# Kernel tuning notes

Hardware: AMD Instinct MI355X
Metric: run time of the kernel (lower is better)

Reference implementation:

```python
import jax, jax.numpy as jnp
import numpy as np

N_NODES = 100000
N_EDGES = 3200000
N_RELS = 8
F_IN = 64
F_OUT = 64


def setup_inputs() -> dict:
    key = jax.random.key(0)
    k1, k2, k3, k4, k5, k6 = jax.random.split(key, 6)
    X = jax.random.normal(k1, (N_NODES, F_IN), dtype=jnp.float32)
    W = jax.random.normal(k2, (N_RELS, F_IN, F_OUT), dtype=jnp.float32) * 0.1
    A = jax.random.uniform(k3, (N_EDGES,), dtype=jnp.float32)
    src = jax.random.randint(k4, (N_EDGES,), 0, N_NODES, dtype=jnp.int32)
    dst = jax.random.randint(k5, (N_EDGES,), 0, N_NODES, dtype=jnp.int32)
    etype = jax.random.randint(k6, (N_EDGES,), 0, N_RELS, dtype=jnp.int32)
    return {"X": X, "W": W, "A": A, "src": src, "dst": dst, "etype": etype}


def reference(X, W, A, src, dst, etype):
    # RGCN hetero forward: Y[i,fo] = sum_{r,j in N_r(i)} A[r,i,j] * (X[j] @ W[r])[fo]
    # Precompute per-relation transformed features: [R, N, F_out]
    XW = jnp.einsum('nf,rfo->rno', X, W)
    # Gather per-edge message and scale by edge weight: [E, F_out]
    msg = XW[etype, src] * A[:, None]
    # Scatter-add into destination nodes: [N, F_out]
    Y = jax.ops.segment_sum(msg, dst, num_segments=X.shape[0])
    return Y
```

## Files before the change

kernel.cpp:

```cpp
#include <hip/hip_runtime.h>
#include <hip/hip_fp16.h>

#define FDIM 64
#define SB 200
#define P_BLK 1024
#define NB_MAX 400
#define BKT_NODES 256
#define CHUNK_CAP 3200

typedef __attribute__((ext_vector_type(8))) short short8;
typedef __attribute__((ext_vector_type(4))) float float4_;

__device__ __forceinline__ unsigned short f2bf(float x) {
    unsigned u = __float_as_uint(x);
    return (unsigned short)((u + 0x7FFF + ((u >> 16) & 1)) >> 16);
}

__global__ __launch_bounds__(256) void xw_gemm_mfma(
    const float* __restrict__ X, const float* __restrict__ Wmat,
    __half* __restrict__ XWh, int N, int R)
{
    __shared__ unsigned short Wt[4 * 64 * 72];
    const int tid  = threadIdx.x;
    const int lane = tid & 63;
    const int wave = tid >> 6;
    const int quad = lane >> 4;
    const int l15  = lane & 15;
    const int blockBase = blockIdx.x * 256;

    short8 bfrag[4][2];
    bool tvalid[4];
#pragma unroll
    for (int t = 0; t < 4; ++t) {
        const int tb = blockBase + (wave * 4 + t) * 16;
        tvalid[t] = (tb < N);
        if (tvalid[t]) {
            const float* xp = X + (size_t)(tb + l15) * FDIM + quad * 8;
            const float4 x0 = *(const float4*)(xp);
            const float4 x1 = *(const float4*)(xp + 4);
            const float4 x2 = *(const float4*)(xp + 32);
            const float4 x3 = *(const float4*)(xp + 36);
            short8 b0, b1;
            b0[0]=f2bf(x0.x); b0[1]=f2bf(x0.y); b0[2]=f2bf(x0.z); b0[3]=f2bf(x0.w);
            b0[4]=f2bf(x1.x); b0[5]=f2bf(x1.y); b0[6]=f2bf(x1.z); b0[7]=f2bf(x1.w);
            b1[0]=f2bf(x2.x); b1[1]=f2bf(x2.y); b1[2]=f2bf(x2.z); b1[3]=f2bf(x2.w);
            b1[4]=f2bf(x3.x); b1[5]=f2bf(x3.y); b1[6]=f2bf(x3.z); b1[7]=f2bf(x3.w);
            bfrag[t][0] = b0; bfrag[t][1] = b1;
        } else {
            bfrag[t][0] = (short8)(0); bfrag[t][1] = (short8)(0);
        }
    }

    for (int rp = 0; rp < 2; ++rp) {
        __syncthreads();
#pragma unroll
        for (int it = 0; it < 16; ++it) {
            const int idx = it * 256 + tid;
            const int k  = idx & 63;
            const int f4 = (idx >> 6) & 15;
            const int r  = idx >> 10;
            const float4 w = *(const float4*)(Wmat + (((size_t)(rp * 4 + r) * FDIM + k) * FDIM + f4 * 4));
            const int base = (r * 64 + f4 * 4) * 72 + k;
            Wt[base + 0 * 72] = f2bf(w.x);
            Wt[base + 1 * 72] = f2bf(w.y);
            Wt[base + 2 * 72] = f2bf(w.z);
            Wt[base + 3 * 72] = f2bf(w.w);
        }
        __syncthreads();

#pragma unroll
        for (int t = 0; t < 4; ++t) {
            if (!tvalid[t]) continue;
            const int tb = blockBase + (wave * 4 + t) * 16;
            const int node = tb + l15;
#pragma unroll
            for (int r = 0; r < 4; ++r) {
                __half* orow = XWh + ((size_t)(rp * 4 + r) * N + node) * FDIM;
#pragma unroll
                for (int ft = 0; ft < 4; ++ft) {
                    const int f = ft * 16 + l15;
                    const unsigned short* wp = &Wt[(r * 64 + f) * 72 + quad * 8];
                    const short8 a0 = *(const short8*)(wp);
                    const short8 a1 = *(const short8*)(wp + 32);
                    float4_ acc = {0.f, 0.f, 0.f, 0.f};
                    acc = __builtin_amdgcn_mfma_f32_16x16x32_bf16(a0, bfrag[t][0], acc, 0, 0, 0);
                    acc = __builtin_amdgcn_mfma_f32_16x16x32_bf16(a1, bfrag[t][1], acc, 0, 0, 0);
                    const __half2 h01 = __floats2half2_rn(acc[0], acc[1]);
                    const __half2 h23 = __floats2half2_rn(acc[2], acc[3]);
                    uint2 st;
                    st.x = *(const unsigned*)&h01;
                    st.y = *(const unsigned*)&h23;
                    *(uint2*)(orow + ft * 16 + quad * 4) = st;
                }
            }
        }
    }
}

__global__ __launch_bounds__(256) void bin_hist(
    const int* __restrict__ dst, int* __restrict__ cnt, int E, int B, int chunk)
{
    __shared__ int lh[NB_MAX];
    const int p = blockIdx.x, tid = threadIdx.x;
    for (int b = tid; b < B; b += 256) lh[b] = 0;
    __syncthreads();
    const int i0 = p * chunk, iend = min(i0 + chunk, E);
    for (int i = i0 + tid; i < iend; i += 256)
        atomicAdd(&lh[dst[i] >> 8], 1);
    __syncthreads();
    for (int b = tid; b < B; b += 256) cnt[(size_t)b * P_BLK + p] = lh[b];
}

__global__ __launch_bounds__(256) void scan_partial(
    const int* __restrict__ cnt, int* __restrict__ blockSums, int M, int CH)
{
    __shared__ int sh[256];
    const int b = blockIdx.x, tid = threadIdx.x;
    const int i0 = b * CH, iend = min(i0 + CH, M);
    int s = 0;
    for (int i = i0 + tid; i < iend; i += 256) s += cnt[i];
    sh[tid] = s; __syncthreads();
    for (int off = 128; off > 0; off >>= 1) {
        if (tid < off) sh[tid] += sh[tid + off];
        __syncthreads();
    }
    if (tid == 0) blockSums[b] = sh[0];
}

__global__ __launch_bounds__(256) void scan_block(int* blockSums, int nb)
{
    __shared__ int sh[256];
    const int tid = threadIdx.x;
    const int v = (tid < nb) ? blockSums[tid] : 0;
    sh[tid] = v; __syncthreads();
    for (int off = 1; off < 256; off <<= 1) {
        const int t = (tid >= off) ? sh[tid - off] : 0;
        __syncthreads();
        sh[tid] += t;
        __syncthreads();
    }
    if (tid < nb) blockSums[tid] = sh[tid] - v;
}

__global__ __launch_bounds__(64) void scan_final(
    const int* __restrict__ cnt, const int* __restrict__ blockSums,
    int* __restrict__ offs, int M, int CH, int E)
{
    const int b = blockIdx.x, lane = threadIdx.x;
    const int i0 = b * CH, iend = min(i0 + CH, M);
    int carry = blockSums[b];
    for (int t = i0; t < iend; t += 64) {
        const int i = t + lane;
        const int c = (i < iend) ? cnt[i] : 0;
        int v = c;
#pragma unroll
        for (int o = 1; o < 64; o <<= 1) {
            const int u = __shfl_up(v, o, 64);
            if (lane >= o) v += u;
        }
        if (i < iend) offs[i] = carry + v - c;
        carry += __shfl(v, 63, 64);
    }
    if (b == (int)gridDim.x - 1 && lane == 0) offs[M] = E;
}

__global__ __launch_bounds__(256) void bin_scatter(
    const int* __restrict__ src, const int* __restrict__ dst,
    const int* __restrict__ etype, const float* __restrict__ A,
    const int* __restrict__ offs, int2* __restrict__ packed,
    int E, int N, int B, int chunk)
{
    __shared__ int lcnt[NB_MAX];
    __shared__ int lpfx[NB_MAX];
    __shared__ int gb[NB_MAX];
    __shared__ int2 recs[CHUNK_CAP];
    __shared__ unsigned short rbkt[CHUNK_CAP];
    const int p = blockIdx.x, tid = threadIdx.x;
    const int i0 = p * chunk, iend = min(i0 + chunk, E);

    for (int b = tid; b < B; b += 256) lcnt[b] = 0;
    __syncthreads();
    for (int i = i0 + tid; i < iend; i += 256)
        atomicAdd(&lcnt[dst[i] >> 8], 1);
    __syncthreads();

    if (tid < 64) {
        int carry = 0;
        for (int t0 = 0; t0 < B; t0 += 64) {
            const int b = t0 + tid;
            const int c = (b < B) ? lcnt[b] : 0;
            int v = c;
#pragma unroll
            for (int o = 1; o < 64; o <<= 1) {
                const int u = __shfl_up(v, o, 64);
                if (tid >= o) v += u;
            }
            if (b < B) lpfx[b] = carry + v - c;
            carry += __shfl(v, 63, 64);
        }
    }
    __syncthreads();
    for (int b = tid; b < B; b += 256) {
        gb[b] = offs[(size_t)b * P_BLK + p] - lpfx[b];
        lcnt[b] = lpfx[b];
    }
    __syncthreads();

    for (int i = i0 + tid; i < iend; i += 256) {
        const int d = dst[i];
        const int b = d >> 8;
        const int slot = atomicAdd(&lcnt[b], 1);
        recs[slot] = make_int2((etype[i] * N + src[i]) | ((d & 255) << 20),
                               __float_as_int(A[i]));
        rbkt[slot] = (unsigned short)b;
    }
    __syncthreads();

    const int tot = iend - i0;
    for (int s = tid; s < tot; s += 256)
        packed[gb[rbkt[s]] + s] = recs[s];
}

__global__ __launch_bounds__(1024) void bucket_sort(
    const int2* __restrict__ packed, const int* __restrict__ offs,
    int2* __restrict__ sorted, int* __restrict__ nodeOffs, int N, int B, int E)
{
    __shared__ int hist[BKT_NODES];
    __shared__ int pfx[BKT_NODES + 1];
    __shared__ int cur[BKT_NODES];
    const int bkt = blockIdx.x, tid = threadIdx.x;
    const int beg = offs[(size_t)bkt * P_BLK];
    const int end = (bkt + 1 < B) ? offs[(size_t)(bkt + 1) * P_BLK] : E;

    if (tid < BKT_NODES) hist[tid] = 0;
    __syncthreads();
    for (int i = beg + tid; i < end; i += 1024)
        atomicAdd(&hist[(packed[i].x >> 20) & (BKT_NODES - 1)], 1);
    __syncthreads();
    if (tid == 0) {
        int s = 0;
        pfx[0] = 0;
        for (int i = 0; i < BKT_NODES; ++i) { s += hist[i]; pfx[i + 1] = s; }
    }
    __syncthreads();
    if (tid < BKT_NODES) {
        cur[tid] = pfx[tid];
        const int n = bkt * BKT_NODES + tid;
        if (n < N) nodeOffs[n] = beg + pfx[tid];
    }
    if (bkt == B - 1 && tid == 0) nodeOffs[N] = E;
    __syncthreads();
    for (int i = beg + tid; i < end; i += 1024) {
        const int2 rec = packed[i];
        const int dl = (rec.x >> 20) & (BKT_NODES - 1);
        const int pos = atomicAdd(&cur[dl], 1);
        sorted[beg + pos] = rec;
    }
}

__global__ __launch_bounds__(256) void dst_aggregate(
    const __half* __restrict__ XWh, const int* __restrict__ nodeOffs,
    const int2* __restrict__ sorted, float* __restrict__ Y, int N)
{
    const int lane = threadIdx.x & 63;
    const int hid  = lane >> 5;
    const int fl   = lane & 31;
    const int wave = (int)((blockIdx.x * blockDim.x + threadIdx.x) >> 6);
    const int nWaves = (int)((gridDim.x * blockDim.x) >> 6);
    const __half2* XW2 = (const __half2*)XWh;

    for (int d = wave; d < N; d += nWaves) {
        const int beg = nodeOffs[d], end = nodeOffs[d + 1];
        float ax = 0.f, ay = 0.f;
        for (int base = beg; base < end; base += 64) {
            const int idx = base + lane;
            const int2 ka = (idx < end) ? sorted[idx] : make_int2(0, 0);
            const int nb = min(64, end - base);
            const int npair = (nb + 1) >> 1;
            int s = 0;
            for (; s + 8 <= npair; s += 8) {
                int k[8], b[8];
#pragma unroll
                for (int u = 0; u < 8; ++u) {
                    const int j = 2 * (s + u) + hid;
                    k[u] = __shfl(ka.x, j, 64);
                    b[u] = __shfl(ka.y, j, 64);
                }
                __half2 v[8];
#pragma unroll
                for (int u = 0; u < 8; ++u)
                    v[u] = XW2[(size_t)(k[u] & 0xFFFFF) * 32 + fl];
#pragma unroll
                for (int u = 0; u < 8; ++u) {
                    const float2 f = __half22float2(v[u]);
                    const float a = __int_as_float(b[u]);
                    ax += a * f.x; ay += a * f.y;
                }
            }
            for (; s < npair; ++s) {
                const int j = 2 * s + hid;
                const int kk = __shfl(ka.x, j, 64);
                const int bb = __shfl(ka.y, j, 64);
                const __half2 v = XW2[(size_t)(kk & 0xFFFFF) * 32 + fl];
                const float2 f = __half22float2(v);
                const float a = __int_as_float(bb);
                ax += a * f.x; ay += a * f.y;
            }
        }
        ax += __shfl_xor(ax, 32, 64);
        ay += __shfl_xor(ay, 32, 64);
        if (lane < 32) {
            ((float2*)(Y + (size_t)d * FDIM))[fl] = make_float2(ax, ay);
        }
    }
}

extern "C" void kernel_launch(void* const* d_in, const int* in_sizes, int n_in,
                              void* d_out, int out_size, void* d_ws, size_t ws_size,
                              hipStream_t stream)
{
    const float* X     = (const float*)d_in[0];
    const float* Wmat  = (const float*)d_in[1];
    const float* A     = (const float*)d_in[2];
    const int*   src   = (const int*)d_in[3];
    const int*   dst   = (const int*)d_in[4];
    const int*   etype = (const int*)d_in[5];
    float* Y = (float*)d_out;

    const int N = in_sizes[0] / FDIM;
    const int R = in_sizes[1] / (FDIM * FDIM);
    const int E = in_sizes[2];
    (void)n_in; (void)out_size; (void)ws_size;

    const int B = (N + BKT_NODES - 1) / BKT_NODES;
    const int M = B * P_BLK;
    const int chunk = (E + P_BLK - 1) / P_BLK;
    const int CH = (M + SB - 1) / SB;

    char* ws = (char*)d_ws;
    size_t off = 0;
    auto take = [&](size_t bytes) { char* p = ws + off; off = (off + bytes + 255) & ~(size_t)255; return p; };
    __half* XWh      = (__half*)take((size_t)R * N * FDIM * sizeof(__half));
    int2*   packed   = (int2*)  take((size_t)E * sizeof(int2));
    int2*   sorted   = (int2*)  take((size_t)E * sizeof(int2));
    int*    cnt      = (int*)   take((size_t)M * sizeof(int));
    int*    offs     = (int*)   take((size_t)(M + 1) * sizeof(int));
    int*    nodeOffs = (int*)   take((size_t)(N + 1) * sizeof(int));
    int*    bsums    = (int*)   take((size_t)SB * sizeof(int));

    xw_gemm_mfma<<<(N + 255) / 256, 256, 0, stream>>>(X, Wmat, XWh, N, R);

    bin_hist<<<P_BLK, 256, 0, stream>>>(dst, cnt, E, B, chunk);
    scan_partial<<<SB, 256, 0, stream>>>(cnt, bsums, M, CH);
    scan_block<<<1, 256, 0, stream>>>(bsums, SB);
    scan_final<<<SB, 64, 0, stream>>>(cnt, bsums, offs, M, CH, E);
    bin_scatter<<<P_BLK, 256, 0, stream>>>(src, dst, etype, A, offs, packed, E, N, B, chunk);
    bucket_sort<<<B, 1024, 0, stream>>>(packed, offs, sorted, nodeOffs, N, B, E);

    dst_aggregate<<<2048, 256, 0, stream>>>(XWh, nodeOffs, sorted, Y, N);
}
```

Measured before the change: 315.6 us.

## Process four edges per wave step with 8-byte gathers and prefetch next node offsets

The aggregation kernel now splits each wave into four 16-lane groups. Each lane loads four fp16 features (a uint2) per edge, so a wave handles four edges per step instead of two, halving the number of gather iterations. The remainder loop is removed by padding the step count to a multiple of 8, relying on the zeroed padding records (weight 0, index 0). The next node's offsets are prefetched during the current node, and the final reduction takes two xor-shuffles across 16-lane groups before a float4 store.

```diff
diff --git a/kernel.cpp b/kernel.cpp
--- a/kernel.cpp
+++ b/kernel.cpp
@@ -263,55 +263,62 @@
     const int2* __restrict__ sorted, float* __restrict__ Y, int N)
 {
     const int lane = threadIdx.x & 63;
-    const int hid  = lane >> 5;
-    const int fl   = lane & 31;
+    const int el   = lane >> 4;
+    const int fl4  = lane & 15;
     const int wave = (int)((blockIdx.x * blockDim.x + threadIdx.x) >> 6);
     const int nWaves = (int)((gridDim.x * blockDim.x) >> 6);
-    const __half2* XW2 = (const __half2*)XWh;
-
-    for (int d = wave; d < N; d += nWaves) {
-        const int beg = nodeOffs[d], end = nodeOffs[d + 1];
-        float ax = 0.f, ay = 0.f;
+    const __half2* __restrict__ XW2 = (const __half2*)XWh;
+    const unsigned foff = (unsigned)(fl4 << 1);
+
+    int d = wave;
+    if (d >= N) return;
+    int beg = nodeOffs[d];
+    int end = nodeOffs[d + 1];
+
+    while (d < N) {
+        const int dn = d + nWaves;
+        int nbeg = 0, nend = 0;
+        if (dn < N) { nbeg = nodeOffs[dn]; nend = nodeOffs[dn + 1]; }
+
+        float4_ acc = {0.f, 0.f, 0.f, 0.f};
         for (int base = beg; base < end; base += 64) {
             const int idx = base + lane;
             const int2 ka = (idx < end) ? sorted[idx] : make_int2(0, 0);
             const int nb = min(64, end - base);
-            const int npair = (nb + 1) >> 1;
-            int s = 0;
-            for (; s + 8 <= npair; s += 8) {
+            const int nsteps = (((nb + 3) >> 2) + 7) & ~7;
+            for (int s = 0; s < nsteps; s += 8) {
                 int k[8], b[8];
 #pragma unroll
                 for (int u = 0; u < 8; ++u) {
-                    const int j = 2 * (s + u) + hid;
+                    const int j = ((s + u) << 2) + el;
                     k[u] = __shfl(ka.x, j, 64);
                     b[u] = __shfl(ka.y, j, 64);
                 }
-                __half2 v[8];
+                uint2 v[8];
 #pragma unroll
                 for (int u = 0; u < 8; ++u)
-                    v[u] = XW2[(size_t)(k[u] & 0xFFFFF) * 32 + fl];
+                    v[u] = *(const uint2*)(XW2 + ((((unsigned)k[u]) & 0xFFFFFu) << 5) + foff);
 #pragma unroll
                 for (int u = 0; u < 8; ++u) {
-                    const float2 f = __half22float2(v[u]);
                     const float a = __int_as_float(b[u]);
-                    ax += a * f.x; ay += a * f.y;
+                    const float2 f0 = __half22float2(*(const __half2*)&v[u].x);
+                    const float2 f1 = __half22float2(*(const __half2*)&v[u].y);
+                    acc[0] += a * f0.x; acc[1] += a * f0.y;
+                    acc[2] += a * f1.x; acc[3] += a * f1.y;
                 }
             }
-            for (; s < npair; ++s) {
-                const int j = 2 * s + hid;
-                const int kk = __shfl(ka.x, j, 64);
-                const int bb = __shfl(ka.y, j, 64);
-                const __half2 v = XW2[(size_t)(kk & 0xFFFFF) * 32 + fl];
-                const float2 f = __half22float2(v);
-                const float a = __int_as_float(bb);
-                ax += a * f.x; ay += a * f.y;
-            }
-        }
-        ax += __shfl_xor(ax, 32, 64);
-        ay += __shfl_xor(ay, 32, 64);
-        if (lane < 32) {
-            ((float2*)(Y + (size_t)d * FDIM))[fl] = make_float2(ax, ay);
-        }
+        }
+#pragma unroll
+        for (int m = 16; m <= 32; m <<= 1) {
+            acc[0] += __shfl_xor(acc[0], m, 64);
+            acc[1] += __shfl_xor(acc[1], m, 64);
+            acc[2] += __shfl_xor(acc[2], m, 64);
+            acc[3] += __shfl_xor(acc[3], m, 64);
+        }
+        if (lane < 16)
+            *(float4_*)(Y + (size_t)d * FDIM + (fl4 << 2)) = acc;
+
+        d = dn; beg = nbeg; end = nend;
     }
 }
 
```

After: 312.4 us. No clear change (-1.0%).
